# Optimization experiments

Measured on AMD Instinct MI355X. Metric: run time of the kernel, lower is better.

The kernel has to match this reference:

```python
import jax, jax.numpy as jnp
import numpy as np

NEG_SLOPE = 0.2
BN_EPS = 1e-5
SM_EPS = 1e-16


def gatv2_conv(x, src, dst, num_nodes, Wl, bl, Wr, br, att, bias, concat):
    # x: [N, Fin]; att: [H, C]
    H, C = att.shape
    xl = (x @ Wl + bl).reshape(-1, H, C)  # source-side (x_j), lin_l
    xr = (x @ Wr + br).reshape(-1, H, C)  # target-side (x_i), lin_r
    e = jax.nn.leaky_relu(xl[src] + xr[dst], NEG_SLOPE)          # [E, H, C]
    logits = jnp.einsum('ehc,hc->eh', e, att)                    # [E, H]
    m = jax.ops.segment_max(logits, dst, num_segments=num_nodes)  # [N, H]
    expv = jnp.exp(logits - m[dst])
    denom = jax.ops.segment_sum(expv, dst, num_segments=num_nodes)
    alpha = expv / (denom[dst] + SM_EPS)                          # [E, H]
    msg = xl[src] * alpha[:, :, None]                             # [E, H, C]
    out = jax.ops.segment_sum(msg, dst, num_segments=num_nodes)   # [N, H, C]
    out = out.reshape(num_nodes, H * C) if concat else out.mean(axis=1)
    return out + bias


def batchnorm(x, gamma, beta):
    mean = x.mean(axis=0)
    var = x.var(axis=0)  # biased, as torch uses for normalization
    return gamma * (x - mean) * jax.lax.rsqrt(var + BN_EPS) + beta


def setup_inputs() -> dict:
    key = jax.random.key(0)
    ks = jax.random.split(key, 16)
    N, E = 50000, 800000
    Fin, Hid, Out, H = 128, 64, 64, 4
    s = 0.05
    inp = {
        'x': jax.random.normal(ks[0], (N, Fin), jnp.float32),
        'edge_index': jax.random.randint(ks[1], (2, E), 0, N, jnp.int64),
        # conv1 (heads=4, concat=False)
        'Wl1': jax.random.normal(ks[2], (Fin, H * Hid), jnp.float32) * s,
        'bl1': jnp.zeros((H * Hid,), jnp.float32),
        'Wr1': jax.random.normal(ks[3], (Fin, H * Hid), jnp.float32) * s,
        'br1': jnp.zeros((H * Hid,), jnp.float32),
        'att1': jax.random.normal(ks[4], (H, Hid), jnp.float32) * s,
        'bias1': jnp.zeros((Hid,), jnp.float32),
        'g1': jnp.ones((Hid,), jnp.float32),
        'beta1': jnp.zeros((Hid,), jnp.float32),
        # conv2 (heads=1, concat=True -> same as single head)
        'Wl2': jax.random.normal(ks[5], (Hid, Out), jnp.float32) * s,
        'bl2': jnp.zeros((Out,), jnp.float32),
        'Wr2': jax.random.normal(ks[6], (Hid, Out), jnp.float32) * s,
        'br2': jnp.zeros((Out,), jnp.float32),
        'att2': jax.random.normal(ks[7], (1, Out), jnp.float32) * s,
        'bias2': jnp.zeros((Out,), jnp.float32),
        'g2': jnp.ones((Out,), jnp.float32),
        'beta2': jnp.zeros((Out,), jnp.float32),
    }
    return inp


def reference(x, edge_index, Wl1, bl1, Wr1, br1, att1, bias1, g1, beta1,
              Wl2, bl2, Wr2, br2, att2, bias2, g2, beta2):
    N = x.shape[0]
    loops = jnp.arange(N, dtype=edge_index.dtype)  # PyG add_self_loops=True
    src = jnp.concatenate([edge_index[0], loops])
    dst = jnp.concatenate([edge_index[1], loops])
    h = gatv2_conv(x, src, dst, N, Wl1, bl1, Wr1, br1, att1, bias1, concat=False)
    h = jax.nn.relu(batchnorm(h, g1, beta1))  # dropout = identity (eval)
    h = gatv2_conv(h, src, dst, N, Wl2, bl2, Wr2, br2, att2, bias2, concat=True)
    h = jax.nn.relu(batchnorm(h, g2, beta2))
    return h
```

## Files before the change

kernel.cpp:

```cpp
#include <hip/hip_runtime.h>
#include <hip/hip_bf16.h>
#include <math.h>

#define TPB 256

typedef __attribute__((ext_vector_type(8))) _Float16 hfrag8;
typedef __attribute__((ext_vector_type(2))) _Float16 h2;
typedef __attribute__((ext_vector_type(4))) float f32x4;

union HU { unsigned int u; h2 h; };
union US8 { unsigned short us[8]; uint4 v; };

static __device__ __forceinline__ h2 as_h2(unsigned int u) { HU c; c.u = u; return c.h; }
static __device__ __forceinline__ unsigned short f2h_bits(float f) {
  union { _Float16 h; unsigned short s; } c; c.h = (_Float16)f; return c.s;
}

#define DPP_ROR(v, C) __int_as_float(__builtin_amdgcn_update_dpp( \
    __float_as_int(v), __float_as_int(v), (C), 0xf, 0xf, false))
static __device__ __forceinline__ float red16(float p) {
  p += DPP_ROR(p, 0x121);
  p += DPP_ROR(p, 0x122);
  p += DPP_ROR(p, 0x124);
  p += DPP_ROR(p, 0x128);
  return p;
}

__global__ void k_deg_wprep(const int* __restrict__ ei, int E, int ET, int* __restrict__ deg,
                            const float* __restrict__ Wl1, const float* __restrict__ Wr1,
                            const float* __restrict__ Wl2, const float* __restrict__ Wr2,
                            unsigned short* __restrict__ wt1l, unsigned short* __restrict__ wt1r,
                            unsigned short* __restrict__ wt2l, unsigned short* __restrict__ wt2r,
                            int egrid) {
  int b = blockIdx.x;
  if (b < egrid) {
    int e = b * TPB + threadIdx.x;
    if (e < ET) {
      int dst = (e < E) ? ei[E + e] : (e - E);
      atomicAdd(&deg[dst], 1);
    }
    return;
  }
  int i = (b - egrid) * TPB + threadIdx.x;
  if (i < 32768) {
    int c = i >> 7, k = i & 127;
    wt1l[i] = f2h_bits(Wl1[(size_t)k * 256 + c]);
  } else if (i < 65536) {
    int j = i - 32768; int c = j >> 7, k = j & 127;
    wt1r[j] = f2h_bits(Wr1[(size_t)k * 256 + c]);
  } else if (i < 69632) {
    int j = i - 65536; int c = j >> 6, k = j & 63;
    wt2l[j] = f2h_bits(Wl2[(size_t)k * 64 + c]);
  } else if (i < 73728) {
    int j = i - 69632; int c = j >> 6, k = j & 63;
    wt2r[j] = f2h_bits(Wr2[(size_t)k * 64 + c]);
  }
}

__global__ void k_scanf(const int* __restrict__ deg, int N,
                        int* __restrict__ rowoff, int* __restrict__ cursor) {
  __shared__ int sm[TPB];
  int t = threadIdx.x;
  int pref = blockIdx.x * TPB;
  int acc = 0;
  for (int j = t; j < pref; j += TPB) acc += (deg[j] + 3) & ~3;
  sm[t] = acc;
  __syncthreads();
  for (int d = TPB / 2; d > 0; d >>= 1) {
    if (t < d) sm[t] += sm[t + d];
    __syncthreads();
  }
  int base = sm[0];
  __syncthreads();
  int i = pref + t;
  int v = (i < N) ? ((deg[i] + 3) & ~3) : 0;
  sm[t] = v;
  __syncthreads();
  for (int d = 1; d < TPB; d <<= 1) {
    int tmp = (t >= d) ? sm[t - d] : 0;
    __syncthreads();
    sm[t] += tmp;
    __syncthreads();
  }
  if (i < N) {
    int off = base + sm[t] - v;
    rowoff[i] = off;
    cursor[i] = off;
  }
}

__global__ void k_fill(const int* __restrict__ ei, int E, int ET, int N,
                       const int* __restrict__ rowoff, const int* __restrict__ deg,
                       int* __restrict__ cursor, int* __restrict__ csrc) {
  int e = blockIdx.x * blockDim.x + threadIdx.x;
  if (e < ET) {
    int src, dst;
    if (e < E) { src = ei[e]; dst = ei[E + e]; } else { src = dst = e - E; }
    csrc[atomicAdd(&cursor[dst], 1)] = src;
  } else {
    int i = e - ET;
    if (i < N) {
      int dg = deg[i];
      int beg = rowoff[i] + dg;
      int end = rowoff[i] + ((dg + 3) & ~3);
      for (int k = beg; k < end; ++k) csrc[k] = 0;
    }
  }
}

__global__ void k_gemm_mfma(const void* __restrict__ Avoid, int af16,
                            const float* __restrict__ affine,
                            const unsigned short* __restrict__ Wt0, const float* __restrict__ b0,
                            const unsigned short* __restrict__ Wt1, const float* __restrict__ b1,
                            unsigned short* __restrict__ out0, unsigned short* __restrict__ out1,
                            int M, int K, int Nc, int mtile, int nt4) {
  extern __shared__ short lds[];
  short* As = lds;
  short* Bls = lds + 64 * K;
  short* Brs = lds + 128 * K;
  int m, nt;
  if (nt4) {
    int xcd = blockIdx.x & 7, gg = blockIdx.x >> 3;
    nt = gg & 3; m = ((gg >> 2) << 3) | xcd;
    if (m >= mtile) return;
  } else {
    m = blockIdx.x; nt = 0;
  }
  const int r0 = m * 64, n0 = nt * 64;
  const int tid = threadIdx.x;
  const int Kb = K * 2;

  if (af16) {
    const unsigned short* A16 = (const unsigned short*)Avoid;
    const int cpr8 = K >> 3;
    for (int idx = tid; idx < 64 * cpr8; idx += TPB) {
      int row = idx / cpr8, k8 = (idx - row * cpr8) * 8;
      int gr = r0 + row;
      uint4 av = make_uint4(0, 0, 0, 0);
      if (gr < M) av = *(const uint4*)(A16 + (size_t)gr * K + k8);
      unsigned int wds[4] = {av.x, av.y, av.z, av.w};
      US8 res;
#pragma unroll
      for (int j = 0; j < 4; ++j) {
        h2 hv = as_h2(wds[j]);
        int c = k8 + j * 2;
        float f0 = fmaxf((float)hv.x * affine[c] + affine[64 + c], 0.f);
        float f1 = fmaxf((float)hv.y * affine[c + 1] + affine[64 + c + 1], 0.f);
        res.us[j * 2] = f2h_bits(f0);
        res.us[j * 2 + 1] = f2h_bits(f1);
      }
      int kb = (k8 * 2) ^ ((row & 7) << 4);
      *(uint4*)((char*)As + row * Kb + kb) = res.v;
    }
  } else {
    const float* A = (const float*)Avoid;
    const int fpr = K >> 2;
    for (int idx = tid; idx < 64 * fpr; idx += TPB) {
      int row = idx / fpr, c4 = idx - row * fpr;
      int gr = r0 + row;
      float4 v = make_float4(0.f, 0.f, 0.f, 0.f);
      if (gr < M) v = *(const float4*)(A + (size_t)gr * K + c4 * 4);
      ushort4 pk;
      pk.x = f2h_bits(v.x); pk.y = f2h_bits(v.y); pk.z = f2h_bits(v.z); pk.w = f2h_bits(v.w);
      int kb = (c4 * 8) ^ ((row & 7) << 4);
      *(ushort4*)((char*)As + row * Kb + kb) = pk;
    }
  }
  const int cpr = K >> 3;
  for (int idx = tid; idx < 64 * cpr; idx += TPB) {
    int c = idx / cpr, k8 = (idx - c * cpr) * 8;
    int kb = (k8 * 2) ^ ((c & 7) << 4);
    uint4 w0 = *(const uint4*)(Wt0 + (size_t)(n0 + c) * K + k8);
    *(uint4*)((char*)Bls + c * Kb + kb) = w0;
    uint4 w1 = *(const uint4*)(Wt1 + (size_t)(n0 + c) * K + k8);
    *(uint4*)((char*)Brs + c * Kb + kb) = w1;
  }
  __syncthreads();

  const int w = tid >> 6, lane = tid & 63;
  const int arow = w * 16 + (lane & 15);
  const int l16 = (lane >> 4) << 3;
  f32x4 accL[4], accR[4];
#pragma unroll
  for (int i = 0; i < 4; ++i) { accL[i] = (f32x4)0.f; accR[i] = (f32x4)0.f; }
  for (int k0 = 0; k0 < K; k0 += 32) {
    int kb = (k0 + l16) * 2;
    hfrag8 af = *(hfrag8*)((char*)As + arow * Kb + (kb ^ ((arow & 7) << 4)));
#pragma unroll
    for (int cf = 0; cf < 4; ++cf) {
      int col = cf * 16 + (lane & 15);
      int cb = col * Kb + (kb ^ ((col & 7) << 4));
      hfrag8 bl = *(hfrag8*)((char*)Bls + cb);
      accL[cf] = __builtin_amdgcn_mfma_f32_16x16x32_f16(af, bl, accL[cf], 0, 0, 0);
      hfrag8 br = *(hfrag8*)((char*)Brs + cb);
      accR[cf] = __builtin_amdgcn_mfma_f32_16x16x32_f16(af, br, accR[cf], 0, 0, 0);
    }
  }
  const int rbase = r0 + w * 16 + ((lane >> 4) << 2);
  const int cbase = n0 + (lane & 15);
#pragma unroll
  for (int cf = 0; cf < 4; ++cf) {
    int gcol = cbase + cf * 16;
    float bb0 = b0[gcol], bb1 = b1[gcol];
#pragma unroll
    for (int r = 0; r < 4; ++r) {
      int grow = rbase + r;
      if (grow < M) {
        out0[(size_t)grow * Nc + gcol] = f2h_bits(accL[cf][r] + bb0);
        out1[(size_t)grow * Nc + gcol] = f2h_bits(accR[cf][r] + bb1);
      }
    }
  }
}

__global__ __launch_bounds__(TPB) void k_gat1(
    const unsigned short* __restrict__ xl, const unsigned short* __restrict__ xr,
    const int* __restrict__ rowoff, const int* __restrict__ deg,
    const int* __restrict__ csrc,
    const float* __restrict__ att, const float* __restrict__ bias,
    unsigned short* __restrict__ out, int N) {
  int node = (blockIdx.x * TPB + threadIdx.x) >> 6;
  int lane = threadIdx.x & 63;
  if (node >= N) return;
  int l4 = lane * 4;
  float4 atv = *(const float4*)(att + l4);
  h2 at01, at23;
  at01.x = (_Float16)atv.x; at01.y = (_Float16)atv.y;
  at23.x = (_Float16)atv.z; at23.y = (_Float16)atv.w;
  float4 bb = *(const float4*)(bias + l4);
  uint2 rv = *(const uint2*)(xr + (node << 8) + l4);
  h2 xr01 = as_h2(rv.x), xr23 = as_h2(rv.y);
  const _Float16 c02 = (_Float16)0.2f;
  int beg = rowoff[node];
  int dg = deg[node];
  int endR = beg + dg;
  int endF = beg + (dg & ~3);
  float s = 0.f, a0 = 0.f, a1 = 0.f, a2 = 0.f, a3 = 0.f;
  int k = beg;
  for (; k < endF; k += 4) {
    int4 q = *(const int4*)(csrc + k);
    uint2 vv[4];
    vv[0] = *(const uint2*)(xl + (q.x << 8) + l4);
    vv[1] = *(const uint2*)(xl + (q.y << 8) + l4);
    vv[2] = *(const uint2*)(xl + (q.z << 8) + l4);
    vv[3] = *(const uint2*)(xl + (q.w << 8) + l4);
    float ps[4];
#pragma unroll
    for (int u = 0; u < 4; ++u) {
      h2 x01 = as_h2(vv[u].x), x23 = as_h2(vv[u].y);
      h2 t01 = x01 + xr01, t23 = x23 + xr23;
      h2 l01 = __builtin_elementwise_max(t01, t01 * c02);
      h2 l23 = __builtin_elementwise_max(t23, t23 * c02);
      ps[u] = __builtin_amdgcn_fdot2(l01, at01,
              __builtin_amdgcn_fdot2(l23, at23, 0.f, false), false);
    }
#pragma unroll
    for (int u = 0; u < 4; ++u) ps[u] = red16(ps[u]);
#pragma unroll
    for (int u = 0; u < 4; ++u) {
      float wv = __expf(ps[u]);
      h2 x01 = as_h2(vv[u].x), x23 = as_h2(vv[u].y);
      s += wv;
      a0 += wv * (float)x01.x; a1 += wv * (float)x01.y;
      a2 += wv * (float)x23.x; a3 += wv * (float)x23.y;
    }
  }
  if (k < endR) {
    int4 q = *(const int4*)(csrc + k);
    uint2 vv[4];
    vv[0] = *(const uint2*)(xl + (q.x << 8) + l4);
    vv[1] = *(const uint2*)(xl + (q.y << 8) + l4);
    vv[2] = *(const uint2*)(xl + (q.z << 8) + l4);
    vv[3] = *(const uint2*)(xl + (q.w << 8) + l4);
    float ps[4];
#pragma unroll
    for (int u = 0; u < 4; ++u) {
      h2 x01 = as_h2(vv[u].x), x23 = as_h2(vv[u].y);
      h2 t01 = x01 + xr01, t23 = x23 + xr23;
      h2 l01 = __builtin_elementwise_max(t01, t01 * c02);
      h2 l23 = __builtin_elementwise_max(t23, t23 * c02);
      ps[u] = __builtin_amdgcn_fdot2(l01, at01,
              __builtin_amdgcn_fdot2(l23, at23, 0.f, false), false);
    }
#pragma unroll
    for (int u = 0; u < 4; ++u) ps[u] = red16(ps[u]);
#pragma unroll
    for (int u = 0; u < 4; ++u) {
      float wv = (k + u < endR) ? __expf(ps[u]) : 0.f;
      h2 x01 = as_h2(vv[u].x), x23 = as_h2(vv[u].y);
      s += wv;
      a0 += wv * (float)x01.x; a1 += wv * (float)x01.y;
      a2 += wv * (float)x23.x; a3 += wv * (float)x23.y;
    }
  }
  float inv = 1.f / (s + 1e-16f);
  a0 *= inv; a1 *= inv; a2 *= inv; a3 *= inv;
  a0 += __shfl_xor(a0, 16); a0 += __shfl_xor(a0, 32);
  a1 += __shfl_xor(a1, 16); a1 += __shfl_xor(a1, 32);
  a2 += __shfl_xor(a2, 16); a2 += __shfl_xor(a2, 32);
  a3 += __shfl_xor(a3, 16); a3 += __shfl_xor(a3, 32);
  if (lane < 16) {
    ushort4 o;
    o.x = f2h_bits(a0 * 0.25f + bb.x);
    o.y = f2h_bits(a1 * 0.25f + bb.y);
    o.z = f2h_bits(a2 * 0.25f + bb.z);
    o.w = f2h_bits(a3 * 0.25f + bb.w);
    *(ushort4*)(out + (node << 6) + l4) = o;
  }
}

__global__ __launch_bounds__(TPB) void k_gat2(
    const unsigned short* __restrict__ xl, const unsigned short* __restrict__ xr,
    const int* __restrict__ rowoff, const int* __restrict__ deg,
    const int* __restrict__ csrc,
    const float* __restrict__ att, const float* __restrict__ bias,
    float* __restrict__ out, int N) {
  int node = (blockIdx.x * TPB + threadIdx.x) >> 6;
  int lane = threadIdx.x & 63;
  if (node >= N) return;
  int grp = lane >> 4, c4 = (lane & 15) * 4;
  float4 atv = *(const float4*)(att + c4);
  h2 at01, at23;
  at01.x = (_Float16)atv.x; at01.y = (_Float16)atv.y;
  at23.x = (_Float16)atv.z; at23.y = (_Float16)atv.w;
  float4 bb = *(const float4*)(bias + c4);
  uint2 rv = *(const uint2*)(xr + (node << 6) + c4);
  h2 xr01 = as_h2(rv.x), xr23 = as_h2(rv.y);
  const _Float16 c02 = (_Float16)0.2f;
  int beg = rowoff[node];
  int dg = deg[node];
  int endR = beg + dg;
  int quads = (dg + 3) >> 2;
  float s = 0.f, a0 = 0.f, a1 = 0.f, a2 = 0.f, a3 = 0.f;
  for (int it = 0; it < quads; ++it) {
    int kk = beg + it * 4 + grp;
    int src = csrc[kk];
    bool ok = kk < endR;
    uint2 v = *(const uint2*)(xl + (src << 6) + c4);
    h2 x01 = as_h2(v.x), x23 = as_h2(v.y);
    h2 t01 = x01 + xr01, t23 = x23 + xr23;
    h2 l01 = __builtin_elementwise_max(t01, t01 * c02);
    h2 l23 = __builtin_elementwise_max(t23, t23 * c02);
    float p = __builtin_amdgcn_fdot2(l01, at01,
              __builtin_amdgcn_fdot2(l23, at23, 0.f, false), false);
    p = red16(p);
    float wv = ok ? __expf(p) : 0.f;
    s += wv;
    a0 += wv * (float)x01.x; a1 += wv * (float)x01.y;
    a2 += wv * (float)x23.x; a3 += wv * (float)x23.y;
  }
  s += __shfl_xor(s, 16); s += __shfl_xor(s, 32);
  a0 += __shfl_xor(a0, 16); a0 += __shfl_xor(a0, 32);
  a1 += __shfl_xor(a1, 16); a1 += __shfl_xor(a1, 32);
  a2 += __shfl_xor(a2, 16); a2 += __shfl_xor(a2, 32);
  a3 += __shfl_xor(a3, 16); a3 += __shfl_xor(a3, 32);
  if (lane < 16) {
    float inv = 1.f / (s + 1e-16f);
    float4 o;
    o.x = a0 * inv + bb.x;
    o.y = a1 * inv + bb.y;
    o.z = a2 * inv + bb.z;
    o.w = a3 * inv + bb.w;
    *(float4*)(out + (node << 6) + c4) = o;
  }
}

__global__ void k_bnstatfin(const void* __restrict__ inv_, int f16in, int N,
                            float* __restrict__ part, int* __restrict__ counter,
                            const float* __restrict__ g, const float* __restrict__ beta,
                            float* __restrict__ ab) {
  __shared__ float sm[TPB], sq[TPB];
  __shared__ float fin[TPB];
  __shared__ int lastsm;
  const float* inf = (const float*)inv_;
  const _Float16* inh = (const _Float16*)inv_;
  int col = threadIdx.x & 63;
  int rq = threadIdx.x >> 6;
  float s0 = 0.f, q0 = 0.f, s1 = 0.f, q1 = 0.f;
  int stride = gridDim.x * 4;
  int r = blockIdx.x * 4 + rq;
  for (; r + stride < N; r += 2 * stride) {
    float v0 = f16in ? (float)inh[(size_t)r * 64 + col] : inf[(size_t)r * 64 + col];
    float v1 = f16in ? (float)inh[(size_t)(r + stride) * 64 + col]
                     : inf[(size_t)(r + stride) * 64 + col];
    s0 += v0; q0 += v0 * v0;
    s1 += v1; q1 += v1 * v1;
  }
  if (r < N) {
    float v0 = f16in ? (float)inh[(size_t)r * 64 + col] : inf[(size_t)r * 64 + col];
    s0 += v0; q0 += v0 * v0;
  }
  sm[threadIdx.x] = s0 + s1; sq[threadIdx.x] = q0 + q1;
  __syncthreads();
  if (threadIdx.x < 128) {
    float v;
    if (threadIdx.x < 64) {
      v = sm[threadIdx.x] + sm[threadIdx.x + 64] + sm[threadIdx.x + 128] + sm[threadIdx.x + 192];
    } else {
      int c = threadIdx.x - 64;
      v = sq[c] + sq[c + 64] + sq[c + 128] + sq[c + 192];
    }
    part[(size_t)blockIdx.x * 128 + threadIdx.x] = v;
  }
  __threadfence();
  __syncthreads();
  if (threadIdx.x == 0) lastsm = atomicAdd(counter, 1);
  __syncthreads();
  if (lastsm != gridDim.x - 1) return;
  __threadfence();
  int t = threadIdx.x;
  int c = t & 127, gidx = t >> 7;
  int B = gridDim.x;
  float acc0 = 0.f, acc1 = 0.f, acc2 = 0.f, acc3 = 0.f;
  int b = gidx;
  for (; b + 6 < B; b += 8) {
    acc0 += part[(size_t)b * 128 + c];
    acc1 += part[(size_t)(b + 2) * 128 + c];
    acc2 += part[(size_t)(b + 4) * 128 + c];
    acc3 += part[(size_t)(b + 6) * 128 + c];
  }
  for (; b < B; b += 2) acc0 += part[(size_t)b * 128 + c];
  fin[t] = (acc0 + acc1) + (acc2 + acc3);
  __syncthreads();
  if (t < 64) {
    float ts = fin[t] + fin[t + 128];
    float tq = fin[t + 64] + fin[t + 192];
    float mean = ts / (float)N;
    float var = tq / (float)N - mean * mean;
    float a = g[t] * rsqrtf(var + 1e-5f);
    ab[t] = a;
    ab[64 + t] = beta[t] - mean * a;
  }
}

__global__ void k_bnapply(const float* __restrict__ in, const float* __restrict__ ab,
                          float* __restrict__ out, int total4) {
  int idx = blockIdx.x * blockDim.x + threadIdx.x;
  if (idx >= total4) return;
  float4 v = *(const float4*)(in + (size_t)idx * 4);
  int c0 = (idx & 15) * 4;
  v.x = fmaxf(v.x * ab[c0 + 0] + ab[64 + c0 + 0], 0.f);
  v.y = fmaxf(v.y * ab[c0 + 1] + ab[64 + c0 + 1], 0.f);
  v.z = fmaxf(v.z * ab[c0 + 2] + ab[64 + c0 + 2], 0.f);
  v.w = fmaxf(v.w * ab[c0 + 3] + ab[64 + c0 + 3], 0.f);
  *(float4*)(out + (size_t)idx * 4) = v;
}

extern "C" void kernel_launch(void* const* d_in, const int* in_sizes, int n_in,
                              void* d_out, int out_size, void* d_ws, size_t ws_size,
                              hipStream_t stream) {
  const float* x     = (const float*)d_in[0];
  const int*   ei    = (const int*)d_in[1];
  const float* Wl1   = (const float*)d_in[2];
  const float* bl1   = (const float*)d_in[3];
  const float* Wr1   = (const float*)d_in[4];
  const float* br1   = (const float*)d_in[5];
  const float* att1  = (const float*)d_in[6];
  const float* bias1 = (const float*)d_in[7];
  const float* g1    = (const float*)d_in[8];
  const float* be1   = (const float*)d_in[9];
  const float* Wl2   = (const float*)d_in[10];
  const float* bl2   = (const float*)d_in[11];
  const float* Wr2   = (const float*)d_in[12];
  const float* br2   = (const float*)d_in[13];
  const float* att2  = (const float*)d_in[14];
  const float* bias2 = (const float*)d_in[15];
  const float* g2    = (const float*)d_in[16];
  const float* be2   = (const float*)d_in[17];
  float* out = (float*)d_out;

  const int N  = in_sizes[0] / 128;
  const int E  = in_sizes[1] / 2;
  const int ET = E + N;
  const int ETP = ET + 4 * ((N + 255) & ~255);
  const int SB = (N + TPB - 1) / TPB;

  char* p = (char*)d_ws;
  auto take = [&](size_t b) { char* q = p; p += (b + 255) & ~(size_t)255; return q; };

  unsigned short* xl1 = (unsigned short*)take((size_t)N * 256 * 2);
  unsigned short* xr1 = (unsigned short*)take((size_t)N * 256 * 2);
  unsigned short* xl2 = (unsigned short*)take((size_t)N * 64 * 2);
  unsigned short* xr2 = (unsigned short*)take((size_t)N * 64 * 2);
  unsigned short* out1 = (unsigned short*)take((size_t)N * 64 * 2);
  unsigned short* wt1l = (unsigned short*)take(256 * 128 * 2);
  unsigned short* wt1r = (unsigned short*)take(256 * 128 * 2);
  unsigned short* wt2l = (unsigned short*)take(64 * 64 * 2);
  unsigned short* wt2r = (unsigned short*)take(64 * 64 * 2);
  int* deg    = (int*)take((size_t)N * 4);
  int* ctr    = (int*)take(512);
  size_t zero_bytes = (char*)ctr + 512 - (char*)deg;
  int* csrc   = (int*)take((size_t)ETP * 4 + 16);
  int* rowoff = (int*)take((size_t)(N + 1) * 4);
  int* cursor = (int*)take((size_t)N * 4);
  float* part = (float*)take((size_t)256 * 128 * 4);
  float* ab1  = (float*)take(128 * 4);
  float* ab2  = (float*)take(128 * 4);
  (void)ws_size; (void)n_in; (void)out_size;

  int egrid = (ET + TPB - 1) / TPB;
  int wgrid = (73728 + TPB - 1) / TPB;
  int fgrid = (ET + N + TPB - 1) / TPB;
  int ngrid = (N + 3) / 4;
  int mtile = (N + 63) / 64;
  int mg8 = (mtile + 7) / 8;
  int total4 = N * 16;

  hipMemsetAsync(deg, 0, zero_bytes, stream);
  k_deg_wprep<<<egrid + wgrid, TPB, 0, stream>>>(ei, E, ET, deg, Wl1, Wr1, Wl2, Wr2,
                                                 wt1l, wt1r, wt2l, wt2r, egrid);
  k_scanf<<<SB, TPB, 0, stream>>>(deg, N, rowoff, cursor);
  k_fill<<<fgrid, TPB, 0, stream>>>(ei, E, ET, N, rowoff, deg, cursor, csrc);

  k_gemm_mfma<<<mg8 * 32, TPB, 3 * 64 * 128 * 2, stream>>>(
      x, 0, nullptr, wt1l, bl1, wt1r, br1, xl1, xr1, N, 128, 256, mtile, 1);
  k_gat1<<<ngrid, TPB, 0, stream>>>(xl1, xr1, rowoff, deg, csrc, att1, bias1, out1, N);
  k_bnstatfin<<<256, TPB, 0, stream>>>(out1, 1, N, part, ctr, g1, be1, ab1);

  k_gemm_mfma<<<mtile, TPB, 3 * 64 * 64 * 2, stream>>>(
      out1, 1, ab1, wt2l, bl2, wt2r, br2, xl2, xr2, N, 64, 64, mtile, 0);
  k_gat2<<<ngrid, TPB, 0, stream>>>(xl2, xr2, rowoff, deg, csrc, att2, bias2, out, N);
  k_bnstatfin<<<256, TPB, 0, stream>>>(out, 0, N, part, ctr + 64, g2, be2, ab2);
  k_bnapply<<<(total4 + TPB - 1) / TPB, TPB, 0, stream>>>(out, ab2, out, total4);
}
```

Measured before the change: 363.7 us.

## Fuse final batchnorm statistics and apply into one grid-synchronized kernel

Merges the second batchnorm statistics kernel and the separate apply kernel into a single kernel. The last block to finish computes the scale and shift and publishes them through a release flag, while the other blocks spin-wait on that flag and then apply normalization and ReLU in place. This removes one launch and the gap between kernels. It relies on all 256 blocks being co-resident so the spin-wait cannot deadlock, and the apply pass re-reads rows each block just touched, which may still be in cache. The first statistics kernel also loses its unused fp32 branch.

```diff
diff --git a/kernel.cpp b/kernel.cpp
--- a/kernel.cpp
+++ b/kernel.cpp
@@ -365,29 +365,27 @@
   }
 }
 
-__global__ void k_bnstatfin(const void* __restrict__ inv_, int f16in, int N,
+__global__ void k_bnstatfin(const unsigned short* __restrict__ inh_, int N,
                             float* __restrict__ part, int* __restrict__ counter,
                             const float* __restrict__ g, const float* __restrict__ beta,
                             float* __restrict__ ab) {
   __shared__ float sm[TPB], sq[TPB];
   __shared__ float fin[TPB];
   __shared__ int lastsm;
-  const float* inf = (const float*)inv_;
-  const _Float16* inh = (const _Float16*)inv_;
+  const _Float16* inh = (const _Float16*)inh_;
   int col = threadIdx.x & 63;
   int rq = threadIdx.x >> 6;
   float s0 = 0.f, q0 = 0.f, s1 = 0.f, q1 = 0.f;
   int stride = gridDim.x * 4;
   int r = blockIdx.x * 4 + rq;
   for (; r + stride < N; r += 2 * stride) {
-    float v0 = f16in ? (float)inh[(size_t)r * 64 + col] : inf[(size_t)r * 64 + col];
-    float v1 = f16in ? (float)inh[(size_t)(r + stride) * 64 + col]
-                     : inf[(size_t)(r + stride) * 64 + col];
+    float v0 = (float)inh[(size_t)r * 64 + col];
+    float v1 = (float)inh[(size_t)(r + stride) * 64 + col];
     s0 += v0; q0 += v0 * v0;
     s1 += v1; q1 += v1 * v1;
   }
   if (r < N) {
-    float v0 = f16in ? (float)inh[(size_t)r * 64 + col] : inf[(size_t)r * 64 + col];
+    float v0 = (float)inh[(size_t)r * 64 + col];
     s0 += v0; q0 += v0 * v0;
   }
   sm[threadIdx.x] = s0 + s1; sq[threadIdx.x] = q0 + q1;
@@ -433,17 +431,84 @@
   }
 }
 
-__global__ void k_bnapply(const float* __restrict__ in, const float* __restrict__ ab,
-                          float* __restrict__ out, int total4) {
-  int idx = blockIdx.x * blockDim.x + threadIdx.x;
-  if (idx >= total4) return;
-  float4 v = *(const float4*)(in + (size_t)idx * 4);
-  int c0 = (idx & 15) * 4;
-  v.x = fmaxf(v.x * ab[c0 + 0] + ab[64 + c0 + 0], 0.f);
-  v.y = fmaxf(v.y * ab[c0 + 1] + ab[64 + c0 + 1], 0.f);
-  v.z = fmaxf(v.z * ab[c0 + 2] + ab[64 + c0 + 2], 0.f);
-  v.w = fmaxf(v.w * ab[c0 + 3] + ab[64 + c0 + 3], 0.f);
-  *(float4*)(out + (size_t)idx * 4) = v;
+__global__ __launch_bounds__(TPB) void k_bn2fused(
+    float* __restrict__ inout, int N, float* __restrict__ part,
+    int* __restrict__ counter, int* __restrict__ flag,
+    const float* __restrict__ g, const float* __restrict__ beta,
+    float* __restrict__ ab) {
+  __shared__ float sm[TPB], sq[TPB];
+  __shared__ float fin[TPB];
+  __shared__ int lastsm;
+  int col = threadIdx.x & 63;
+  int rq = threadIdx.x >> 6;
+  float s0 = 0.f, q0 = 0.f, s1 = 0.f, q1 = 0.f;
+  int stride = gridDim.x * 4;
+  int r0 = blockIdx.x * 4 + rq;
+  for (int r = r0; r < N; r += 2 * stride) {
+    float v0 = inout[(size_t)r * 64 + col];
+    s0 += v0; q0 += v0 * v0;
+    int r2 = r + stride;
+    if (r2 < N) {
+      float v1 = inout[(size_t)r2 * 64 + col];
+      s1 += v1; q1 += v1 * v1;
+    }
+  }
+  sm[threadIdx.x] = s0 + s1; sq[threadIdx.x] = q0 + q1;
+  __syncthreads();
+  if (threadIdx.x < 128) {
+    float v;
+    if (threadIdx.x < 64) {
+      v = sm[threadIdx.x] + sm[threadIdx.x + 64] + sm[threadIdx.x + 128] + sm[threadIdx.x + 192];
+    } else {
+      int c = threadIdx.x - 64;
+      v = sq[c] + sq[c + 64] + sq[c + 128] + sq[c + 192];
+    }
+    part[(size_t)blockIdx.x * 128 + threadIdx.x] = v;
+  }
+  __threadfence();
+  __syncthreads();
+  if (threadIdx.x == 0) lastsm = atomicAdd(counter, 1);
+  __syncthreads();
+  if (lastsm == gridDim.x - 1) {
+    __threadfence();
+    int t = threadIdx.x;
+    int c = t & 127, gidx = t >> 7;
+    int B = gridDim.x;
+    float acc0 = 0.f, acc1 = 0.f, acc2 = 0.f, acc3 = 0.f;
+    int b = gidx;
+    for (; b + 6 < B; b += 8) {
+      acc0 += part[(size_t)b * 128 + c];
+      acc1 += part[(size_t)(b + 2) * 128 + c];
+      acc2 += part[(size_t)(b + 4) * 128 + c];
+      acc3 += part[(size_t)(b + 6) * 128 + c];
+    }
+    for (; b < B; b += 2) acc0 += part[(size_t)b * 128 + c];
+    fin[t] = (acc0 + acc1) + (acc2 + acc3);
+    __syncthreads();
+    if (t < 64) {
+      float ts = fin[t] + fin[t + 128];
+      float tq = fin[t + 64] + fin[t + 192];
+      float mean = ts / (float)N;
+      float var = tq / (float)N - mean * mean;
+      float a = g[t] * rsqrtf(var + 1e-5f);
+      ab[t] = a;
+      ab[64 + t] = beta[t] - mean * a;
+    }
+    __syncthreads();
+    __threadfence();
+    if (t == 0) __hip_atomic_store(flag, 1, __ATOMIC_RELEASE, __HIP_MEMORY_SCOPE_AGENT);
+  } else {
+    if (threadIdx.x == 0) {
+      while (__hip_atomic_load(flag, __ATOMIC_ACQUIRE, __HIP_MEMORY_SCOPE_AGENT) == 0)
+        __builtin_amdgcn_s_sleep(8);
+    }
+    __syncthreads();
+  }
+  float ac = ab[col], bc = ab[64 + col];
+  for (int r = r0; r < N; r += stride) {
+    size_t idx = (size_t)r * 64 + col;
+    inout[idx] = fmaxf(inout[idx] * ac + bc, 0.f);
+  }
 }
 
 extern "C" void kernel_launch(void* const* d_in, const int* in_sizes, int n_in,
@@ -488,8 +553,8 @@
   unsigned short* wt2l = (unsigned short*)take(64 * 64 * 2);
   unsigned short* wt2r = (unsigned short*)take(64 * 64 * 2);
   int* deg    = (int*)take((size_t)N * 4);
-  int* ctr    = (int*)take(512);
-  size_t zero_bytes = (char*)ctr + 512 - (char*)deg;
+  int* ctr    = (int*)take(1024);
+  size_t zero_bytes = (char*)ctr + 1024 - (char*)deg;
   int* csrc   = (int*)take((size_t)ETP * 4 + 16);
   int* rowoff = (int*)take((size_t)(N + 1) * 4);
   int* cursor = (int*)take((size_t)N * 4);
@@ -504,7 +569,6 @@
   int ngrid = (N + 3) / 4;
   int mtile = (N + 63) / 64;
   int mg8 = (mtile + 7) / 8;
-  int total4 = N * 16;
 
   hipMemsetAsync(deg, 0, zero_bytes, stream);
   k_deg_wprep<<<egrid + wgrid, TPB, 0, stream>>>(ei, E, ET, deg, Wl1, Wr1, Wl2, Wr2,
@@ -515,11 +579,10 @@
   k_gemm_mfma<<<mg8 * 32, TPB, 3 * 64 * 128 * 2, stream>>>(
       x, 0, nullptr, wt1l, bl1, wt1r, br1, xl1, xr1, N, 128, 256, mtile, 1);
   k_gat1<<<ngrid, TPB, 0, stream>>>(xl1, xr1, rowoff, deg, csrc, att1, bias1, out1, N);
-  k_bnstatfin<<<256, TPB, 0, stream>>>(out1, 1, N, part, ctr, g1, be1, ab1);
+  k_bnstatfin<<<256, TPB, 0, stream>>>(out1, N, part, ctr, g1, be1, ab1);
 
   k_gemm_mfma<<<mtile, TPB, 3 * 64 * 64 * 2, stream>>>(
       out1, 1, ab1, wt2l, bl2, wt2r, br2, xl2, xr2, N, 64, 64, mtile, 0);
   k_gat2<<<ngrid, TPB, 0, stream>>>(xl2, xr2, rowoff, deg, csrc, att2, bias2, out, N);
-  k_bnstatfin<<<256, TPB, 0, stream>>>(out, 0, N, part, ctr + 64, g2, be2, ab2);
-  k_bnapply<<<(total4 + TPB - 1) / TPB, TPB, 0, stream>>>(out, ab2, out, total4);
-}
+  k_bn2fused<<<256, TPB, 0, stream>>>(out, N, part, ctr + 64, ctr + 128, g2, be2, ab2);
+}
```

Measured after the change: 437.3 us. +20.2%, slower.
